# Performance work log

Hardware: AMD Instinct MI355X
Metric: run time of the kernel (lower is better)

## Reference

```python
import jax, jax.numpy as jnp
import numpy as np

B, S, D, H = 2, 2048, 1024, 16
HD = D // H  # head_dim = 64
ROPE_BASE = 10000.0


def _rope_cos_sin(seq_len, head_dim, dtype=jnp.float32):
    inv_freq = 1.0 / (ROPE_BASE ** (jnp.arange(0, head_dim, 2, dtype=jnp.float32) / head_dim))
    t = jnp.arange(seq_len, dtype=jnp.float32)
    freqs = jnp.einsum('i,j->ij', t, inv_freq)          # [S, HD/2]
    emb = jnp.concatenate([freqs, freqs], axis=-1)       # [S, HD]
    return jnp.cos(emb).astype(dtype), jnp.sin(emb).astype(dtype)


def _rotate_half(x):
    x1, x2 = jnp.split(x, 2, axis=-1)
    return jnp.concatenate([-x2, x1], axis=-1)


def setup_inputs() -> dict:
    key = jax.random.key(0)
    ks = jax.random.split(key, 5)
    scale = 1.0 / np.sqrt(D)
    return {
        'hidden_states': jax.random.normal(ks[0], (B, S, D), dtype=jnp.float32),
        'Wq': jax.random.normal(ks[1], (D, D), dtype=jnp.float32) * scale,
        'Wk': jax.random.normal(ks[2], (D, D), dtype=jnp.float32) * scale,
        'Wv': jax.random.normal(ks[3], (D, D), dtype=jnp.float32) * scale,
        'Wo': jax.random.normal(ks[4], (D, D), dtype=jnp.float32) * scale,
    }


def reference(hidden_states, Wq, Wk, Wv, Wo):
    b, s, d = hidden_states.shape
    # torch nn.Linear(weight W) computes x @ W^T
    q = hidden_states @ Wq.T
    k = hidden_states @ Wk.T
    v = hidden_states @ Wv.T
    # [B, H, S, HD]
    q = q.reshape(b, s, H, HD).transpose(0, 2, 1, 3)
    k = k.reshape(b, s, H, HD).transpose(0, 2, 1, 3)
    v = v.reshape(b, s, H, HD).transpose(0, 2, 1, 3)
    cos, sin = _rope_cos_sin(s, HD, q.dtype)  # [S, HD]
    cos = cos[None, None]  # [1,1,S,HD]
    sin = sin[None, None]
    q = q * cos + _rotate_half(q) * sin
    k = k * cos + _rotate_half(k) * sin
    scale = HD ** -0.5
    attn = jnp.einsum('bhqd,bhkd->bhqk', q, k) * scale
    attn = jax.nn.softmax(attn.astype(jnp.float32), axis=-1).astype(q.dtype)
    out = jnp.einsum('bhqk,bhkd->bhqd', attn, v)
    out = out.transpose(0, 2, 1, 3).reshape(b, s, d)
    return out @ Wo.T
```

## Files before the change

kernel.cpp:

```cpp
#include <hip/hip_runtime.h>
#include <math.h>

constexpr int Bc = 2;
constexpr int Sc = 2048;
constexpr int Dc = 1024;
constexpr int Hc = 16;
constexpr int HDc = 64;

constexpr float QSC = 0.125f * 1.4426950408889634f;

typedef __attribute__((ext_vector_type(8))) short bf16x8;
typedef __attribute__((ext_vector_type(4))) float f32x4;
typedef __attribute__((ext_vector_type(4))) unsigned short us4;
typedef __attribute__((ext_vector_type(2))) unsigned int u32x2;
typedef __attribute__((ext_vector_type(4))) unsigned int u32x4;

__device__ __forceinline__ unsigned f2bf(float x) {
    unsigned u = __float_as_uint(x);
    return (u + 0x7FFFu + ((u >> 16) & 1u)) >> 16;
}

__device__ __forceinline__ void split2(float x, unsigned short& h, unsigned short& l) {
    unsigned hh = f2bf(x);
    h = (unsigned short)hh;
    l = (unsigned short)f2bf(x - __uint_as_float(hh << 16));
}

#if __has_builtin(__builtin_amdgcn_permlane32_swap)
__device__ __forceinline__ void plswap32(unsigned& a, unsigned& b) {
    u32x2 r = __builtin_amdgcn_permlane32_swap(a, b, false, false);
    a = r.x; b = r.y;
}
#else
__device__ __forceinline__ void plswap32(unsigned& a, unsigned& b) {
    asm volatile("v_permlane32_swap_b32 %0, %1" : "+v"(a), "+v"(b));
}
#endif
#if __has_builtin(__builtin_amdgcn_permlane16_swap)
__device__ __forceinline__ void plswap16(unsigned& a, unsigned& b) {
    u32x2 r = __builtin_amdgcn_permlane16_swap(a, b, false, false);
    a = r.x; b = r.y;
}
#else
__device__ __forceinline__ void plswap16(unsigned& a, unsigned& b) {
    asm volatile("v_permlane16_swap_b32 %0, %1" : "+v"(a), "+v"(b));
}
#endif

__device__ __forceinline__ void exppack(const f32x4& sv, unsigned& w0, unsigned& w1) {
    unsigned u0 = __float_as_uint(__builtin_amdgcn_exp2f(sv[0]));
    unsigned u1 = __float_as_uint(__builtin_amdgcn_exp2f(sv[1]));
    unsigned u2 = __float_as_uint(__builtin_amdgcn_exp2f(sv[2]));
    unsigned u3 = __float_as_uint(__builtin_amdgcn_exp2f(sv[3]));
    w0 = __builtin_amdgcn_perm(u1, u0, 0x07060302u);
    w1 = __builtin_amdgcn_perm(u3, u2, 0x07060302u);
}

__global__ void rope_table(float* __restrict__ ct, float* __restrict__ st_) {
    int id = blockIdx.x * 256 + threadIdx.x;
    int s = id >> 5;
    int i = id & 31;
    double invf = pow(10000.0, -(double)i / 32.0);
    double ang = (double)s * invf;
    ct[id] = (float)cos(ang);
    st_[id] = (float)sin(ang);
}

__global__ void split_xw(const float* __restrict__ x,
                         const float* __restrict__ Wq, const float* __restrict__ Wk,
                         const float* __restrict__ Wv, const float* __restrict__ Wo,
                         unsigned short* __restrict__ xh,
                         unsigned short* __restrict__ whAll, unsigned short* __restrict__ wlAll) {
    int y = blockIdx.y;
    const float* src;
    unsigned short* h;
    unsigned short* l = nullptr;
    int n;
    if (y == 0) { src = x; h = xh; n = 1 << 22; }
    else {
        src = (y == 1) ? Wq : (y == 2) ? Wk : (y == 3) ? Wv : Wo;
        h = whAll + (size_t)(y - 1) * (1 << 20);
        if (y == 4) l = wlAll + (size_t)3 * (1 << 20);
        n = 1 << 20;
    }
    int i = (blockIdx.x * 256 + threadIdx.x) * 4;
    if (i >= n) return;
    float4 v = *(const float4*)(src + i);
    us4 hh;
    ((unsigned short*)&hh)[0] = (unsigned short)f2bf(v.x);
    ((unsigned short*)&hh)[1] = (unsigned short)f2bf(v.y);
    ((unsigned short*)&hh)[2] = (unsigned short)f2bf(v.z);
    ((unsigned short*)&hh)[3] = (unsigned short)f2bf(v.w);
    *(us4*)(h + i) = hh;
    if (l) {
        us4 ll;
        const float* vp = (const float*)&v;
#pragma unroll
        for (int e = 0; e < 4; e++) {
            unsigned short hi = ((unsigned short*)&hh)[e];
            ((unsigned short*)&ll)[e] =
                (unsigned short)f2bf(vp[e] - __uint_as_float((unsigned)hi << 16));
        }
        *(us4*)(l + i) = ll;
    }
}

__global__ __launch_bounds__(512, 4) void gemm_qkv(
    const unsigned short* __restrict__ Ah,
    const unsigned short* __restrict__ whAll,
    unsigned short* __restrict__ Qh,
    unsigned short* __restrict__ Kh,
    unsigned short* __restrict__ Vh,
    const float* __restrict__ ct, const float* __restrict__ st_) {
    constexpr int K = 1024;
    __shared__ __align__(16) unsigned short As[2 * 4096], Bs[2 * 4096];

    const int z = blockIdx.z;
    const unsigned short* Wh = whAll + (size_t)z * (1 << 20);

    const int t = threadIdx.x;
    const int lane = t & 63;
    const int wave = t >> 6;
    const int l = lane & 15;
    const int quad = lane >> 4;
    const int wr = wave >> 1;
    const int wc = wave & 1;
    const int m0 = blockIdx.x * 128;
    const int n0 = blockIdx.y * 128;

    const int arow = t & 127, akc = t >> 7;
    const unsigned short* gA = Ah + (size_t)(m0 + arow) * K + akc * 8;
    const unsigned short* gB = Wh + (size_t)(n0 + arow) * K + akc * 8;

    f32x4 acc[2][4];
#pragma unroll
    for (int i = 0; i < 2; i++)
#pragma unroll
        for (int j = 0; j < 4; j++) acc[i][j] = (f32x4){0.f, 0.f, 0.f, 0.f};

    __builtin_amdgcn_global_load_lds(
        (const __attribute__((address_space(1))) unsigned int*)gA,
        (__attribute__((address_space(3))) unsigned int*)(As + t * 8), 16, 0, 0);
    __builtin_amdgcn_global_load_lds(
        (const __attribute__((address_space(1))) unsigned int*)gB,
        (__attribute__((address_space(3))) unsigned int*)(Bs + t * 8), 16, 0, 0);

    for (int it = 0; it < 32; ++it) {
        __syncthreads();
        if (it + 1 < 32) {
            const int koff = (it + 1) * 32;
            const int bo = ((it + 1) & 1) * 4096;
            __builtin_amdgcn_global_load_lds(
                (const __attribute__((address_space(1))) unsigned int*)(gA + koff),
                (__attribute__((address_space(3))) unsigned int*)(As + bo + t * 8), 16, 0, 0);
            __builtin_amdgcn_global_load_lds(
                (const __attribute__((address_space(1))) unsigned int*)(gB + koff),
                (__attribute__((address_space(3))) unsigned int*)(Bs + bo + t * 8), 16, 0, 0);
        }
        const unsigned short* a = As + (it & 1) * 4096;
        const unsigned short* bb = Bs + (it & 1) * 4096;
        bf16x8 ah[2], bh[4];
#pragma unroll
        for (int i = 0; i < 2; i++)
            ah[i] = *(const bf16x8*)&a[(quad * 128 + wr * 32 + i * 16 + l) * 8];
#pragma unroll
        for (int j = 0; j < 4; j++)
            bh[j] = *(const bf16x8*)&bb[(quad * 128 + wc * 64 + j * 16 + l) * 8];
#pragma unroll
        for (int i = 0; i < 2; i++)
#pragma unroll
            for (int j = 0; j < 4; j++)
                acc[i][j] = __builtin_amdgcn_mfma_f32_16x16x32_bf16(ah[i], bh[j], acc[i][j], 0, 0, 0);
    }

    const int hcol = blockIdx.y * 2 + wc;
    if (z == 2) {
#pragma unroll
        for (int i = 0; i < 2; i++) {
            int m_base = m0 + wr * 32 + i * 16 + quad * 4;
            int bbk = m_base >> 11;
            int T = (m_base & (Sc - 1)) >> 6;
            int ii = (2 * wr + i) & 3;
            int kk = ii >> 1;
            int qd = ((ii & 1) << 1) | (quad >> 1);
            int tj = (quad & 1) * 4;
            size_t tilebase = (((size_t)(bbk * Hc + hcol)) * 32 + T) * 4096;
#pragma unroll
            for (int jj = 0; jj < 4; jj++) {
                int d = jj * 16 + l;
                size_t off = tilebase + (size_t)(((kk * 4 + qd) * 64 + d) * 8 + tj);
                us4 v4;
#pragma unroll
                for (int r = 0; r < 4; r++)
                    ((unsigned short*)&v4)[r] = (unsigned short)f2bf(acc[i][jj][r]);
                *(us4*)(Vh + off) = v4;
            }
        }
    } else {
#pragma unroll
        for (int i = 0; i < 2; i++)
#pragma unroll
            for (int r = 0; r < 4; r++) {
                int m = m0 + wr * 32 + i * 16 + quad * 4 + r;
                int bbk = m >> 11, s = m & (Sc - 1);
#pragma unroll
                for (int jp = 0; jp < 2; jp++) {
                    int d = jp * 16 + l;
                    float cs = ct[s * 32 + d];
                    float sn = st_[s * 32 + d];
                    float x0 = acc[i][jp][r];
                    float x1 = acc[i][jp + 2][r];
                    float y0 = x0 * cs - x1 * sn;
                    float y1 = x1 * cs + x0 * sn;
                    if (z == 0) {
                        size_t rowb = (((size_t)(bbk * Hc + hcol)) * Sc + s) * HDc;
                        Qh[rowb + d]      = (unsigned short)f2bf(y0 * QSC);
                        Qh[rowb + d + 32] = (unsigned short)f2bf(y1 * QSC);
                    } else {
                        int T = s >> 6, tok = s & 63;
                        size_t tb = (((size_t)(bbk * Hc + hcol)) * 32 + T) * 8;
                        size_t off0 = ((tb + (d >> 3)) * 64 + tok) * 8 + (d & 7);
                        size_t off1 = ((tb + (d >> 3) + 4) * 64 + tok) * 8 + (d & 7);
                        Kh[off0] = (unsigned short)f2bf(y0);
                        Kh[off1] = (unsigned short)f2bf(y1);
                    }
                }
            }
    }
}

__global__ __launch_bounds__(512) void attn10(
    const unsigned short* __restrict__ Qh,
    const unsigned short* __restrict__ Kh,
    const unsigned short* __restrict__ Vh,
    unsigned short* __restrict__ AOh, unsigned short* __restrict__ AOl) {
    __shared__ __align__(16) unsigned short KsH[3 * 4096], VtH[3 * 4096];

    const int t = threadIdx.x;
    const int lane = t & 63;
    const int wave = t >> 6;
    const int l = lane & 15;
    const int quad = lane >> 4;
    const int id = blockIdx.x;
    const int bh = (id & 7) * 4 + (id >> 6);
    const int qt = (id >> 3) & 7;
    const int q0 = qt * 256;
    const int b = bh >> 4;
    const int hh = bh & 15;

    const bf16x8 ONES8 = {(short)0x3F80, (short)0x3F80, (short)0x3F80, (short)0x3F80,
                          (short)0x3F80, (short)0x3F80, (short)0x3F80, (short)0x3F80};

    bf16x8 qf[2][2];
#pragma unroll
    for (int bnd = 0; bnd < 2; bnd++) {
        size_t rowb = ((size_t)bh * Sc + q0 + wave * 32 + bnd * 16 + l) * HDc;
#pragma unroll
        for (int ks = 0; ks < 2; ks++)
            qf[bnd][ks] = *(const bf16x8*)(Qh + rowb + ks * 32 + quad * 8);
    }

    f32x4 o[2][4], lac[2];
#pragma unroll
    for (int bnd = 0; bnd < 2; bnd++) {
        lac[bnd] = (f32x4){0.f, 0.f, 0.f, 0.f};
#pragma unroll
        for (int i = 0; i < 4; i++) o[bnd][i] = (f32x4){0.f, 0.f, 0.f, 0.f};
    }

    const int tensor = wave >> 2;
    const int coff0 = (wave * 2) & 7;
    unsigned short* larr = tensor ? VtH : KsH;
    const unsigned short* gT =
        (tensor ? Vh : Kh) + (size_t)bh * Sc * HDc + coff0 * 512 + lane * 8;

#pragma unroll
    for (int q = 0; q < 2; q++)
        __builtin_amdgcn_global_load_lds(
            (const __attribute__((address_space(1))) unsigned int*)(gT + q * 512),
            (__attribute__((address_space(3))) unsigned int*)(larr + coff0 * 512 + q * 512),
            16, 0, 0);

    int bc = 0;
    for (int kt = 0; kt < 32; kt++) {
        if (kt + 1 < 32) {
            int nb = bc + 1; if (nb == 3) nb = 0;
            const unsigned short* g = gT + (size_t)(kt + 1) * 4096;
            unsigned short* dst = larr + nb * 4096 + coff0 * 512;
#pragma unroll
            for (int q = 0; q < 2; q++)
                __builtin_amdgcn_global_load_lds(
                    (const __attribute__((address_space(1))) unsigned int*)(g + q * 512),
                    (__attribute__((address_space(3))) unsigned int*)(dst + q * 512),
                    16, 0, 0);
            asm volatile("s_waitcnt vmcnt(2)" ::: "memory");
        } else {
            asm volatile("s_waitcnt vmcnt(0)" ::: "memory");
        }
        __builtin_amdgcn_s_barrier();
        const unsigned short* Kbuf = KsH + bc * 4096;
        const unsigned short* Vbuf = VtH + bc * 4096;

        f32x4 s[2][4];
#pragma unroll
        for (int bnd = 0; bnd < 2; bnd++)
#pragma unroll
            for (int tt = 0; tt < 4; tt++) s[bnd][tt] = (f32x4){0.f, 0.f, 0.f, 0.f};
        __builtin_amdgcn_s_setprio(1);
#pragma unroll
        for (int ks = 0; ks < 2; ks++)
#pragma unroll
            for (int tt = 0; tt < 4; tt++) {
                bf16x8 kf = *(const bf16x8*)&Kbuf[((ks * 4 + quad) * 64 + tt * 16 + l) * 8];
                s[0][tt] = __builtin_amdgcn_mfma_f32_16x16x32_bf16(kf, qf[0][ks], s[0][tt], 0, 0, 0);
                s[1][tt] = __builtin_amdgcn_mfma_f32_16x16x32_bf16(kf, qf[1][ks], s[1][tt], 0, 0, 0);
            }
        __builtin_amdgcn_s_setprio(0);

        bf16x8 pf[2][2];
#pragma unroll
        for (int bnd = 0; bnd < 2; bnd++)
#pragma unroll
            for (int ttp = 0; ttp < 2; ttp++) {
                unsigned A0, A1, B0, B1;
                exppack(s[bnd][2 * ttp], A0, A1);
                exppack(s[bnd][2 * ttp + 1], B0, B1);
                plswap32(A0, B0);
                plswap16(A0, B0);
                plswap32(A1, B1);
                plswap16(A1, B1);
                u32x4 fw = {A0, A1, B0, B1};
                bf16x8 p8 = __builtin_bit_cast(bf16x8, fw);
                pf[bnd][ttp] = p8;
                lac[bnd] = __builtin_amdgcn_mfma_f32_16x16x32_bf16(ONES8, p8, lac[bnd], 0, 0, 0);
            }

        __builtin_amdgcn_s_setprio(1);
#pragma unroll
        for (int kk = 0; kk < 2; kk++)
#pragma unroll
            for (int dd = 0; dd < 4; dd++) {
                bf16x8 vf = *(const bf16x8*)
                    &Vbuf[(size_t)((kk * 4 + quad) * 64 + dd * 16 + l) * 8];
                o[0][dd] = __builtin_amdgcn_mfma_f32_16x16x32_bf16(vf, pf[0][kk], o[0][dd], 0, 0, 0);
                o[1][dd] = __builtin_amdgcn_mfma_f32_16x16x32_bf16(vf, pf[1][kk], o[1][dd], 0, 0, 0);
            }
        __builtin_amdgcn_s_setprio(0);
        if (++bc == 3) bc = 0;
    }

#pragma unroll
    for (int bnd = 0; bnd < 2; bnd++) {
        float inv = 1.f / lac[bnd][0];
        int q = q0 + wave * 32 + bnd * 16 + l;
        size_t rowb = ((size_t)b * Sc + q) * Dc + hh * HDc + quad * 4;
#pragma unroll
        for (int dd = 0; dd < 4; dd++) {
            us4 h4, l4;
#pragma unroll
            for (int r = 0; r < 4; r++)
                split2(o[bnd][dd][r] * inv,
                       ((unsigned short*)&h4)[r], ((unsigned short*)&l4)[r]);
            *(us4*)(AOh + rowb + dd * 16) = h4;
            *(us4*)(AOl + rowb + dd * 16) = l4;
        }
    }
}

__global__ __launch_bounds__(512, 2) void gemm_out(
    const unsigned short* __restrict__ Ah, const unsigned short* __restrict__ Al,
    const unsigned short* __restrict__ Wh, const unsigned short* __restrict__ Wl,
    float* __restrict__ C) {
    constexpr int K = 1024;
    __shared__ __align__(16) unsigned short AsH[3 * 4096], AsL[3 * 4096],
                                            BsH[3 * 4096], BsL[3 * 4096];

    const int t = threadIdx.x;
    const int lane = t & 63;
    const int wave = t >> 6;
    const int l = lane & 15;
    const int quad = lane >> 4;
    const int wr = wave >> 1;
    const int wc = wave & 1;
    const int m0 = blockIdx.x * 128;
    const int n0 = blockIdx.y * 128;

    const int arow = t & 127, akc = t >> 7;
    const unsigned short* gah = Ah + (size_t)(m0 + arow) * K + akc * 8;
    const unsigned short* gal = Al + (size_t)(m0 + arow) * K + akc * 8;
    const unsigned short* gbh = Wh + (size_t)(n0 + arow) * K + akc * 8;
    const unsigned short* gbl = Wl + (size_t)(n0 + arow) * K + akc * 8;

    f32x4 acc[2][4];
#pragma unroll
    for (int i = 0; i < 2; i++)
#pragma unroll
        for (int j = 0; j < 4; j++) acc[i][j] = (f32x4){0.f, 0.f, 0.f, 0.f};

#define STAGE_OUT(koff, bo)                                                                \
    do {                                                                                   \
        __builtin_amdgcn_global_load_lds(                                                  \
            (const __attribute__((address_space(1))) unsigned int*)(gah + (koff)),         \
            (__attribute__((address_space(3))) unsigned int*)(AsH + (bo) + t * 8), 16, 0, 0); \
        __builtin_amdgcn_global_load_lds(                                                  \
            (const __attribute__((address_space(1))) unsigned int*)(gal + (koff)),         \
            (__attribute__((address_space(3))) unsigned int*)(AsL + (bo) + t * 8), 16, 0, 0); \
        __builtin_amdgcn_global_load_lds(                                                  \
            (const __attribute__((address_space(1))) unsigned int*)(gbh + (koff)),         \
            (__attribute__((address_space(3))) unsigned int*)(BsH + (bo) + t * 8), 16, 0, 0); \
        __builtin_amdgcn_global_load_lds(                                                  \
            (const __attribute__((address_space(1))) unsigned int*)(gbl + (koff)),         \
            (__attribute__((address_space(3))) unsigned int*)(BsL + (bo) + t * 8), 16, 0, 0); \
    } while (0)

    STAGE_OUT(0, 0);

    int bc = 0;
    for (int it = 0; it < 32; ++it) {
        if (it + 1 < 32) {
            int nb = bc + 1; if (nb == 3) nb = 0;
            STAGE_OUT((it + 1) * 32, nb * 4096);
            asm volatile("s_waitcnt vmcnt(4)" ::: "memory");
        } else {
            asm volatile("s_waitcnt vmcnt(0)" ::: "memory");
        }
        __builtin_amdgcn_s_barrier();
        const int bo = bc * 4096;
        bf16x8 ah[2], al[2], bh[4], bl[4];
#pragma unroll
        for (int i = 0; i < 2; i++) {
            int ra = bo + (quad * 128 + wr * 32 + i * 16 + l) * 8;
            ah[i] = *(const bf16x8*)&AsH[ra];
            al[i] = *(const bf16x8*)&AsL[ra];
        }
#pragma unroll
        for (int j = 0; j < 4; j++) {
            int rb = bo + (quad * 128 + wc * 64 + j * 16 + l) * 8;
            bh[j] = *(const bf16x8*)&BsH[rb];
            bl[j] = *(const bf16x8*)&BsL[rb];
        }
#pragma unroll
        for (int i = 0; i < 2; i++)
#pragma unroll
            for (int j = 0; j < 4; j++) {
                acc[i][j] = __builtin_amdgcn_mfma_f32_16x16x32_bf16(ah[i], bh[j], acc[i][j], 0, 0, 0);
                acc[i][j] = __builtin_amdgcn_mfma_f32_16x16x32_bf16(al[i], bh[j], acc[i][j], 0, 0, 0);
                acc[i][j] = __builtin_amdgcn_mfma_f32_16x16x32_bf16(ah[i], bl[j], acc[i][j], 0, 0, 0);
            }
        if (++bc == 3) bc = 0;
    }
#undef STAGE_OUT

#pragma unroll
    for (int i = 0; i < 2; i++)
#pragma unroll
        for (int j = 0; j < 4; j++)
#pragma unroll
            for (int r = 0; r < 4; r++) {
                int m = m0 + wr * 32 + i * 16 + quad * 4 + r;
                int n = n0 + wc * 64 + j * 16 + l;
                C[(size_t)m * Dc + n] = acc[i][j][r];
            }
}

extern "C" void kernel_launch(void* const* d_in, const int* in_sizes, int n_in,
                              void* d_out, int out_size, void* d_ws, size_t ws_size,
                              hipStream_t stream) {
    const float* x  = (const float*)d_in[0];
    const float* Wq = (const float*)d_in[1];
    const float* Wk = (const float*)d_in[2];
    const float* Wv = (const float*)d_in[3];
    const float* Wo = (const float*)d_in[4];
    float* out = (float*)d_out;

    unsigned short* usw = (unsigned short*)d_ws;
    const size_t M4 = (size_t)1 << 22;
    unsigned short* whAll = usw;
    unsigned short* wlAll = usw + M4;
    unsigned short* xh = usw + 2 * M4;
    unsigned short* xl = usw + 3 * M4;
    unsigned short* Qh = usw + 4 * M4;
    unsigned short* Kh = usw + 5 * M4;
    unsigned short* Vh = usw + 6 * M4;
    float* ct = (float*)(usw + 7 * M4);
    float* st_ = ct + (size_t)Sc * 32;
    unsigned short* AOh = xh;
    unsigned short* AOl = xl;

    rope_table<<<dim3((Sc * 32) / 256), dim3(256), 0, stream>>>(ct, st_);
    split_xw<<<dim3(4096, 5), dim3(256), 0, stream>>>(x, Wq, Wk, Wv, Wo, xh, whAll, wlAll);
    gemm_qkv<<<dim3(32, 8, 3), dim3(512), 0, stream>>>(
        xh, whAll, Qh, Kh, Vh, ct, st_);
    attn10<<<dim3(256), dim3(512), 0, stream>>>(Qh, Kh, Vh, AOh, AOl);
    gemm_out<<<dim3(32, 8), dim3(512), 0, stream>>>(
        AOh, AOl, whAll + 3 * (1 << 20), wlAll + 3 * (1 << 20), out);
}
```

Measured before the change: 238.7 us.

## Split-K the output projection GEMM in two and add partials

The output projection GEMM is split along K into two halves over a new grid z dimension. The 256 tiles of the old grid become 512, giving more parallelism on a GPU with many CUs. Each half writes its own fp32 partial, one into the output and one into the reused Q buffer, and a new add_partial kernel sums them. The LDS ring shrinks from triple to double buffering with a plain __syncthreads, and launch bounds request 4 blocks per CU. The cost is an extra kernel launch, a 16 MB partial write and read, and less load/compute overlap in the main loop.

```diff
diff --git a/kernel.cpp b/kernel.cpp
--- a/kernel.cpp
+++ b/kernel.cpp
@@ -367,13 +367,13 @@
     }
 }
 
-__global__ __launch_bounds__(512, 2) void gemm_out(
+__global__ __launch_bounds__(512, 4) void gemm_out(
     const unsigned short* __restrict__ Ah, const unsigned short* __restrict__ Al,
     const unsigned short* __restrict__ Wh, const unsigned short* __restrict__ Wl,
-    float* __restrict__ C) {
+    float* __restrict__ C0, float* __restrict__ C1) {
     constexpr int K = 1024;
-    __shared__ __align__(16) unsigned short AsH[3 * 4096], AsL[3 * 4096],
-                                            BsH[3 * 4096], BsL[3 * 4096];
+    __shared__ __align__(16) unsigned short AsH[2 * 4096], AsL[2 * 4096],
+                                            BsH[2 * 4096], BsL[2 * 4096];
 
     const int t = threadIdx.x;
     const int lane = t & 63;
@@ -384,12 +384,14 @@
     const int wc = wave & 1;
     const int m0 = blockIdx.x * 128;
     const int n0 = blockIdx.y * 128;
+    const int k0 = blockIdx.z * 512;
+    float* __restrict__ C = blockIdx.z ? C1 : C0;
 
     const int arow = t & 127, akc = t >> 7;
-    const unsigned short* gah = Ah + (size_t)(m0 + arow) * K + akc * 8;
-    const unsigned short* gal = Al + (size_t)(m0 + arow) * K + akc * 8;
-    const unsigned short* gbh = Wh + (size_t)(n0 + arow) * K + akc * 8;
-    const unsigned short* gbl = Wl + (size_t)(n0 + arow) * K + akc * 8;
+    const unsigned short* gah = Ah + (size_t)(m0 + arow) * K + k0 + akc * 8;
+    const unsigned short* gal = Al + (size_t)(m0 + arow) * K + k0 + akc * 8;
+    const unsigned short* gbh = Wh + (size_t)(n0 + arow) * K + k0 + akc * 8;
+    const unsigned short* gbl = Wl + (size_t)(n0 + arow) * K + k0 + akc * 8;
 
     f32x4 acc[2][4];
 #pragma unroll
@@ -415,17 +417,10 @@
 
     STAGE_OUT(0, 0);
 
-    int bc = 0;
-    for (int it = 0; it < 32; ++it) {
-        if (it + 1 < 32) {
-            int nb = bc + 1; if (nb == 3) nb = 0;
-            STAGE_OUT((it + 1) * 32, nb * 4096);
-            asm volatile("s_waitcnt vmcnt(4)" ::: "memory");
-        } else {
-            asm volatile("s_waitcnt vmcnt(0)" ::: "memory");
-        }
-        __builtin_amdgcn_s_barrier();
-        const int bo = bc * 4096;
+    for (int it = 0; it < 16; ++it) {
+        __syncthreads();
+        if (it + 1 < 16) STAGE_OUT((it + 1) * 32, ((it + 1) & 1) * 4096);
+        const int bo = (it & 1) * 4096;
         bf16x8 ah[2], al[2], bh[4], bl[4];
 #pragma unroll
         for (int i = 0; i < 2; i++) {
@@ -447,7 +442,6 @@
                 acc[i][j] = __builtin_amdgcn_mfma_f32_16x16x32_bf16(al[i], bh[j], acc[i][j], 0, 0, 0);
                 acc[i][j] = __builtin_amdgcn_mfma_f32_16x16x32_bf16(ah[i], bl[j], acc[i][j], 0, 0, 0);
             }
-        if (++bc == 3) bc = 0;
     }
 #undef STAGE_OUT
 
@@ -461,6 +455,14 @@
                 int n = n0 + wc * 64 + j * 16 + l;
                 C[(size_t)m * Dc + n] = acc[i][j][r];
             }
+}
+
+__global__ void add_partial(float* __restrict__ out, const float* __restrict__ p1) {
+    int i = (blockIdx.x * 256 + threadIdx.x) * 4;
+    float4 a = *(const float4*)(out + i);
+    float4 b = *(const float4*)(p1 + i);
+    a.x += b.x; a.y += b.y; a.z += b.z; a.w += b.w;
+    *(float4*)(out + i) = a;
 }
 
 extern "C" void kernel_launch(void* const* d_in, const int* in_sizes, int n_in,
@@ -486,12 +488,14 @@
     float* st_ = ct + (size_t)Sc * 32;
     unsigned short* AOh = xh;
     unsigned short* AOl = xl;
+    float* P1 = (float*)Qh;
 
     rope_table<<<dim3((Sc * 32) / 256), dim3(256), 0, stream>>>(ct, st_);
     split_xw<<<dim3(4096, 5), dim3(256), 0, stream>>>(x, Wq, Wk, Wv, Wo, xh, whAll, wlAll);
     gemm_qkv<<<dim3(32, 8, 3), dim3(512), 0, stream>>>(
         xh, whAll, Qh, Kh, Vh, ct, st_);
     attn10<<<dim3(256), dim3(512), 0, stream>>>(Qh, Kh, Vh, AOh, AOl);
-    gemm_out<<<dim3(32, 8), dim3(512), 0, stream>>>(
-        AOh, AOl, whAll + 3 * (1 << 20), wlAll + 3 * (1 << 20), out);
-}
+    gemm_out<<<dim3(32, 8, 2), dim3(512), 0, stream>>>(
+        AOh, AOl, whAll + 3 * (1 << 20), wlAll + 3 * (1 << 20), out, P1);
+    add_partial<<<dim3(4096), dim3(256), 0, stream>>>(out, P1);
+}
```

Measured after the change: 229.4 us. -3.9%, faster.
